# Performance work log

Hardware: AMD Instinct MI355X
Metric: run time of the kernel (lower is better)

The kernel has to match this reference:

```python
import jax, jax.numpy as jnp
import numpy as np
import math

B, C, H, W = 64, 32, 80, 80
HEADS, HD = 8, 4
L = H * W
INV_PI = 1.0 / math.pi


def _conv2d(x, w, pad):
    return jax.lax.conv_general_dilated(x, w, (1, 1), pad, dimension_numbers=('NCHW', 'OIHW', 'NCHW'))


def _lin_angular(x, qkv_w, proj_w, proj_b, dconv_w):
    # x: (B, L, C) -> softmax-free angular linear attention
    qkv = (x @ qkv_w.T).reshape(B, L, 3, HEADS, HD).transpose(2, 0, 3, 1, 4)
    q, k, v = qkv[0], qkv[1], qkv[2]  # (B, HEADS, L, HD)
    q = q / jnp.linalg.norm(q, axis=-1, keepdims=True)
    k = k / jnp.linalg.norm(k, axis=-1, keepdims=True)
    # depthwise conv over L with kernel (9,1), one channel per head
    dconv_v = jax.lax.conv_general_dilated(v, dconv_w, (1, 1), ((4, 4), (0, 0)),
                                           feature_group_count=HEADS,
                                           dimension_numbers=('NCHW', 'OIHW', 'NCHW'))
    attn = jnp.einsum('bhld,bhle->bhde', k, v)  # (B,H,HD,HD)
    out = 0.5 * v + INV_PI * jnp.einsum('bhld,bhde->bhle', q, attn)
    out = out / jnp.linalg.norm(out, axis=-1, keepdims=True)
    out = out + dconv_v
    out = out.transpose(0, 2, 1, 3).reshape(B, L, C)
    return out @ proj_w.T + proj_b


def _xca(x, qkv_w, temp, proj_w, proj_b):
    # x: (B, L, C) -> cross-covariance (channel) attention
    qkv = (x @ qkv_w.T).reshape(B, L, 3, HEADS, HD).transpose(2, 0, 3, 4, 1)
    q, k, v = qkv[0], qkv[1], qkv[2]  # (B, HEADS, HD, L)
    q = q / jnp.maximum(jnp.linalg.norm(q, axis=-1, keepdims=True), 1e-12)
    k = k / jnp.maximum(jnp.linalg.norm(k, axis=-1, keepdims=True), 1e-12)
    attn = jax.nn.softmax(jnp.einsum('bhdn,bhen->bhde', q, k) * temp, axis=-1)
    out = jnp.einsum('bhde,bhen->bhdn', attn, v)  # (B,H,HD,L)
    out = out.transpose(0, 3, 1, 2).reshape(B, L, C)
    return out @ proj_w.T + proj_b


def _chan_vec(f, wa, ba, wa2, ba2, wm, bm, wm2, bm2):
    # f: (B, C, L) -> (B, C, 1) pooled channel descriptor (avg + max branches)
    avg = f.mean(axis=-1)  # (B, C)
    mx = f.max(axis=-1)    # (B, C)
    a = jax.nn.relu(avg @ wa.T + ba) @ wa2.T + ba2
    m = jax.nn.relu(mx @ wm.T + bm) @ wm2.T + bm2
    return (a + m)[..., None]  # (B, C, 1)


def _spatial_gate(a, c1w, c1b, c2w, c2b):
    # a: (B, C, L) -> (B, 1, L) softmax spatial gate
    am = a.reshape(B, C, H, W)
    pooled = jnp.concatenate([am.mean(axis=1, keepdims=True), am.max(axis=1, keepdims=True)], axis=1)
    y = jax.nn.relu(_conv2d(pooled, c1w, ((1, 1), (1, 1))) + c1b[None, :, None, None])
    y = _conv2d(y, c2w, ((1, 1), (1, 1))) + c2b[None, :, None, None]
    return jax.nn.softmax(y.reshape(B, 1, L), axis=-1)


def _forward(rgb, freq, la_qkv_w, la_proj_w, la_proj_b, la_dconv_w,
             xa_qkv_w, xa_temp, xa_proj_w, xa_proj_b,
             c1s_w, c1s_b, c2s_w, c2s_b,
             avg1_w, avg1_b, max1_w, max1_b, avg2_w, avg2_b, max2_w, max2_b,
             avg11_w, avg11_b, max11_w, max11_b, avg22_w, avg22_b, max22_w, max22_b):
    x1 = rgb.reshape(B, C, L).transpose(0, 2, 1)  # to_3d: (B, L, C)
    la1 = _lin_angular(x1, la_qkv_w, la_proj_w, la_proj_b, la_dconv_w)
    x2 = freq.reshape(B, C, L).transpose(0, 2, 1)
    xa1 = _xca(x2, xa_qkv_w, xa_temp, xa_proj_w, xa_proj_b)
    # CAFM works on flattened (B, C, L)
    f1 = la1.transpose(0, 2, 1)
    f2 = xa1.transpose(0, 2, 1)
    a1 = _chan_vec(f1, avg1_w, avg1_b, avg11_w, avg11_b, max1_w, max1_b, max11_w, max11_b)
    a2 = _chan_vec(f2, avg2_w, avg2_b, avg22_w, avg22_b, max2_w, max2_b, max22_w, max22_b)
    cross = jnp.einsum('bci,bdi->bcd', a1, a2)  # (B, C, C)
    a1f = jnp.einsum('bcd,bdl->bcl', jax.nn.softmax(cross, axis=-1), f1)
    a2f = jnp.einsum('bcd,bdl->bcl', jax.nn.softmax(cross.transpose(0, 2, 1), axis=-1), f2)
    g1 = _spatial_gate(a1f, c1s_w, c1s_b, c2s_w, c2s_b)
    g2 = _spatial_gate(a2f, c1s_w, c1s_b, c2s_w, c2s_b)
    f1 = f1 * g1 + f1
    f2 = f2 * g2 + f2
    # torch: (B,C,L).transpose(0,1) -> (C,B,L); sum; permute(1,2,0) -> (B,L,C); to_4d -> (B,C,H,W)
    # transposes cancel: equivalent to (f1+f2).reshape(B, C, H, W)
    return (f1 + f2).reshape(B, C, H, W)


def setup_inputs() -> dict:
    key = jax.random.key(0)
    ks = iter(jax.random.split(key, 40))
    def rn(shape, s=0.05):
        return jax.random.normal(next(ks), shape, dtype=jnp.float32) * s
    return dict(
        rgb=jax.random.normal(next(ks), (B, C, H, W), dtype=jnp.float32),
        freq=jax.random.normal(next(ks), (B, C, H, W), dtype=jnp.float32),
        la_qkv_w=rn((3 * C, C)), la_proj_w=rn((C, C)), la_proj_b=jnp.zeros((C,), jnp.float32),
        la_dconv_w=rn((HEADS, 1, 9, 1)),
        xa_qkv_w=rn((3 * C, C)), xa_temp=jnp.ones((HEADS, 1, 1), jnp.float32),
        xa_proj_w=rn((C, C)), xa_proj_b=jnp.zeros((C,), jnp.float32),
        c1s_w=rn((1, 2, 3, 3)), c1s_b=jnp.zeros((1,), jnp.float32),
        c2s_w=rn((1, 1, 3, 3)), c2s_b=jnp.zeros((1,), jnp.float32),
        avg1_w=rn((16, C)), avg1_b=jnp.zeros((16,), jnp.float32),
        max1_w=rn((16, C)), max1_b=jnp.zeros((16,), jnp.float32),
        avg2_w=rn((16, C)), avg2_b=jnp.zeros((16,), jnp.float32),
        max2_w=rn((16, C)), max2_b=jnp.zeros((16,), jnp.float32),
        avg11_w=rn((C, 16)), avg11_b=jnp.zeros((C,), jnp.float32),
        max11_w=rn((C, 16)), max11_b=jnp.zeros((C,), jnp.float32),
        avg22_w=rn((C, 16)), avg22_b=jnp.zeros((C,), jnp.float32),
        max22_w=rn((C, 16)), max22_b=jnp.zeros((C,), jnp.float32),
    )


def reference(rgb, freq, la_qkv_w, la_proj_w, la_proj_b, la_dconv_w,
              xa_qkv_w, xa_temp, xa_proj_w, xa_proj_b,
              c1s_w, c1s_b, c2s_w, c2s_b,
              avg1_w, avg1_b, max1_w, max1_b, avg2_w, avg2_b, max2_w, max2_b,
              avg11_w, avg11_b, max11_w, max11_b, avg22_w, avg22_b, max22_w, max22_b):
    return _forward(rgb, freq, la_qkv_w, la_proj_w, la_proj_b, la_dconv_w,
                    xa_qkv_w, xa_temp, xa_proj_w, xa_proj_b,
                    c1s_w, c1s_b, c2s_w, c2s_b,
                    avg1_w, avg1_b, max1_w, max1_b, avg2_w, avg2_b, max2_w, max2_b,
                    avg11_w, avg11_b, max11_w, max11_b, avg22_w, avg22_b, max22_w, max22_b)
```

## Files before the change

kernel.cpp:

```cpp
#include <hip/hip_runtime.h>

#define BN 64
#define CN 32
#define HEADSN 8
#define HDN 4
#define LN 6400
#define CL (CN*LN)


__device__ __forceinline__ unsigned fenc(float f){
  unsigned u = __float_as_uint(f);
  return (u & 0x80000000u) ? ~u : (u | 0x80000000u);
}
__device__ __forceinline__ float fdec(unsigned u){
  unsigned v = (u & 0x80000000u) ? (u & 0x7FFFFFFFu) : ~u;
  return __uint_as_float(v);
}

template<bool MAXOP>
__device__ __forceinline__ float bfly32(const float* in, int lane, int* chOut){
  const bool h0 = (lane & 1)  != 0, h1 = (lane & 2)  != 0, h2 = (lane & 4) != 0,
             h3 = (lane & 8)  != 0, h4 = (lane & 16) != 0;
  float a[16];
  #pragma unroll
  for (int i = 0; i < 16; ++i){
    float send = h0 ? in[i] : in[i+16];
    float keep = h0 ? in[i+16] : in[i];
    float recv = __shfl_xor(send, 1, 64);
    a[i] = MAXOP ? fmaxf(keep, recv) : keep + recv;
  }
  float b[8];
  #pragma unroll
  for (int i = 0; i < 8; ++i){
    float send = h1 ? a[i] : a[i+8];
    float keep = h1 ? a[i+8] : a[i];
    float recv = __shfl_xor(send, 2, 64);
    b[i] = MAXOP ? fmaxf(keep, recv) : keep + recv;
  }
  float c[4];
  #pragma unroll
  for (int i = 0; i < 4; ++i){
    float send = h2 ? b[i] : b[i+4];
    float keep = h2 ? b[i+4] : b[i];
    float recv = __shfl_xor(send, 4, 64);
    c[i] = MAXOP ? fmaxf(keep, recv) : keep + recv;
  }
  float d[2];
  #pragma unroll
  for (int i = 0; i < 2; ++i){
    float send = h3 ? c[i] : c[i+2];
    float keep = h3 ? c[i+2] : c[i];
    float recv = __shfl_xor(send, 8, 64);
    d[i] = MAXOP ? fmaxf(keep, recv) : keep + recv;
  }
  float e;
  {
    float send = h4 ? d[0] : d[1];
    float keep = h4 ? d[1] : d[0];
    float recv = __shfl_xor(send, 16, 64);
    e = MAXOP ? fmaxf(keep, recv) : keep + recv;
  }
  {
    float recv = __shfl_xor(e, 32, 64);
    e = MAXOP ? fmaxf(e, recv) : e + recv;
  }
  *chOut = (h0?16:0)|(h1?8:0)|(h2?4:0)|(h3?2:0)|(h4?1:0);
  return e;
}

__device__ __forceinline__ float bfly16_sum(const float* in, int lane, int* chOut){
  const bool h0 = (lane & 1) != 0, h1 = (lane & 2) != 0, h2 = (lane & 4) != 0,
             h3 = (lane & 8) != 0;
  float a[8];
  #pragma unroll
  for (int i = 0; i < 8; ++i){
    float send = h0 ? in[i] : in[i+8];
    float keep = h0 ? in[i+8] : in[i];
    float recv = __shfl_xor(send, 1, 64);
    a[i] = keep + recv;
  }
  float b[4];
  #pragma unroll
  for (int i = 0; i < 4; ++i){
    float send = h1 ? a[i] : a[i+4];
    float keep = h1 ? a[i+4] : a[i];
    float recv = __shfl_xor(send, 2, 64);
    b[i] = keep + recv;
  }
  float c[2];
  #pragma unroll
  for (int i = 0; i < 2; ++i){
    float send = h2 ? b[i] : b[i+2];
    float keep = h2 ? b[i+2] : b[i];
    float recv = __shfl_xor(send, 4, 64);
    c[i] = keep + recv;
  }
  float e;
  {
    float send = h3 ? c[0] : c[1];
    float keep = h3 ? c[1] : c[0];
    float recv = __shfl_xor(send, 8, 64);
    e = keep + recv;
  }
  e += __shfl_xor(e, 16, 64);
  e += __shfl_xor(e, 32, 64);
  *chOut = (h0?8:0)|(h1?4:0)|(h2?2:0)|(h3?1:0);
  return e;
}

__global__ __launch_bounds__(256, 4) void k_la_reduce(const float* __restrict__ rgb,
                                                      const float* __restrict__ Wqkv,
                                                      float* __restrict__ la_attn){
  __shared__ float2 xs2[256*17];
  const int b = blockIdx.y, l0 = blockIdx.x*256, tid = threadIdx.x;
  const float* xg = rgb + (size_t)b*CL + l0;
  #pragma unroll
  for (int c2 = 0; c2 < 16; ++c2){
    float e0 = xg[(2*c2)*LN + tid];
    float e1 = xg[(2*c2+1)*LN + tid];
    xs2[tid*17 + c2] = make_float2(e0, e1);
  }
  __syncthreads();
  const int wave = __builtin_amdgcn_readfirstlane(tid >> 6);
  const int lane = tid & 63;
  const float* Wk = Wqkv + (32 + wave*8)*32;
  const float* Wv = Wqkv + (64 + wave*8)*32;
  float acc[32];
  #pragma unroll
  for (int i = 0; i < 32; ++i) acc[i] = 0.f;
  for (int it = 0; it < 4; ++it){
    const int ll = it*64 + lane;
    float xv[32];
    #pragma unroll
    for (int c2 = 0; c2 < 16; ++c2){
      float2 t = xs2[ll*17 + c2];
      xv[2*c2] = t.x; xv[2*c2+1] = t.y;
    }
    float kk[8], vv[8];
    #pragma unroll
    for (int r = 0; r < 8; ++r){ kk[r] = 0.f; vv[r] = 0.f; }
    #pragma unroll
    for (int c = 0; c < 32; ++c){
      #pragma unroll
      for (int r = 0; r < 8; ++r){
        kk[r] = fmaf(Wk[r*32 + c], xv[c], kk[r]);
        vv[r] = fmaf(Wv[r*32 + c], xv[c], vv[r]);
      }
    }
    #pragma unroll
    for (int hh = 0; hh < 2; ++hh){
      const float* k = kk + hh*4;
      const float* v = vv + hh*4;
      float rn = rsqrtf(k[0]*k[0] + k[1]*k[1] + k[2]*k[2] + k[3]*k[3]);
      #pragma unroll
      for (int d = 0; d < 4; ++d){
        float kn = k[d]*rn;
        #pragma unroll
        for (int e = 0; e < 4; ++e)
          acc[hh*16 + d*4 + e] = fmaf(kn, v[e], acc[hh*16 + d*4 + e]);
      }
    }
  }
  int ch;
  float s = bfly32<false>(acc, lane, &ch);
  if (lane < 32) atomicAdd(la_attn + b*128 + wave*32 + ch, s);
}

__global__ __launch_bounds__(256, 4) void k_xa_reduce(const float* __restrict__ freq,
                                                      const float* __restrict__ Wqkv,
                                                      float* __restrict__ xa_sums){
  __shared__ float2 xs2[256*17];
  const int b = blockIdx.y, l0 = blockIdx.x*256, tid = threadIdx.x;
  const float* xg = freq + (size_t)b*CL + l0;
  #pragma unroll
  for (int c2 = 0; c2 < 16; ++c2){
    float e0 = xg[(2*c2)*LN + tid];
    float e1 = xg[(2*c2+1)*LN + tid];
    xs2[tid*17 + c2] = make_float2(e0, e1);
  }
  __syncthreads();
  const int wave = __builtin_amdgcn_readfirstlane(tid >> 6);
  const int lane = tid & 63;
  const float* Wq = Wqkv + (0  + wave*8)*32;
  const float* Wk = Wqkv + (32 + wave*8)*32;
  float acc[48];
  #pragma unroll
  for (int i = 0; i < 48; ++i) acc[i] = 0.f;
  for (int it = 0; it < 4; ++it){
    const int ll = it*64 + lane;
    float xv[32];
    #pragma unroll
    for (int c2 = 0; c2 < 16; ++c2){
      float2 t = xs2[ll*17 + c2];
      xv[2*c2] = t.x; xv[2*c2+1] = t.y;
    }
    float qq[8], kk[8];
    #pragma unroll
    for (int r = 0; r < 8; ++r){ qq[r] = 0.f; kk[r] = 0.f; }
    #pragma unroll
    for (int c = 0; c < 32; ++c){
      #pragma unroll
      for (int r = 0; r < 8; ++r){
        qq[r] = fmaf(Wq[r*32 + c], xv[c], qq[r]);
        kk[r] = fmaf(Wk[r*32 + c], xv[c], kk[r]);
      }
    }
    #pragma unroll
    for (int hh = 0; hh < 2; ++hh){
      const float* q = qq + hh*4;
      const float* k = kk + hh*4;
      const int base = hh*24;
      #pragma unroll
      for (int d = 0; d < 4; ++d){
        #pragma unroll
        for (int e = 0; e < 4; ++e)
          acc[base + d*4 + e] = fmaf(q[d], k[e], acc[base + d*4 + e]);
      }
      #pragma unroll
      for (int d = 0; d < 4; ++d) acc[base + 16 + d] = fmaf(q[d], q[d], acc[base + 16 + d]);
      #pragma unroll
      for (int e = 0; e < 4; ++e) acc[base + 20 + e] = fmaf(k[e], k[e], acc[base + 20 + e]);
    }
  }
  float* dst = xa_sums + b*192 + wave*48;
  int ch;
  float s0 = bfly32<false>(acc, lane, &ch);
  if (lane < 32) atomicAdd(dst + ch, s0);
  int ch2;
  float s1 = bfly16_sum(acc + 32, lane, &ch2);
  if (lane < 16) atomicAdd(dst + 32 + ch2, s1);
}

__global__ __launch_bounds__(64) void k_fold(const float* __restrict__ xa_sums,
                                             const float* __restrict__ temp,
                                             const float* __restrict__ Wqkv,
                                             const float* __restrict__ Wp,
                                             float* __restrict__ M2){
  __shared__ float attn_s[128];
  const int b = blockIdx.x, t = threadIdx.x;
  if (t < 32){
    const int h = t >> 2, d = t & 3;
    const float* xss = xa_sums + b*192 + h*24;
    const float tmp = temp[h];
    const float nq = fmaxf(sqrtf(xss[16 + d]), 1e-12f);
    float lg[4]; float m = -1e30f;
    #pragma unroll
    for (int e = 0; e < 4; ++e){
      float nk = fmaxf(sqrtf(xss[20 + e]), 1e-12f);
      lg[e] = xss[d*4 + e] * tmp / (nq*nk);
      m = fmaxf(m, lg[e]);
    }
    float Z = 0.f;
    #pragma unroll
    for (int e = 0; e < 4; ++e){ lg[e] = __expf(lg[e] - m); Z += lg[e]; }
    float iZ = 1.f/Z;
    #pragma unroll
    for (int e = 0; e < 4; ++e) attn_s[h*16 + d*4 + e] = lg[e]*iZ;
  }
  __syncthreads();
  if (t < 32){
    const int c = t;
    const float* Wv = Wqkv + 64*32;
    float tmpv[32];
    #pragma unroll
    for (int k = 0; k < 32; ++k){
      const int h = k >> 2, d = k & 3;
      float s = 0.f;
      #pragma unroll
      for (int e = 0; e < 4; ++e)
        s = fmaf(attn_s[h*16 + d*4 + e], Wv[(h*4 + e)*32 + c], s);
      tmpv[k] = s;
    }
    float out[32];
    #pragma unroll
    for (int r = 0; r < 32; ++r) out[r] = 0.f;
    #pragma unroll
    for (int k = 0; k < 32; ++k){
      #pragma unroll
      for (int r = 0; r < 32; ++r)
        out[r] = fmaf(Wp[r*32 + k], tmpv[k], out[r]);
    }
    #pragma unroll
    for (int r = 0; r < 32; ++r) M2[b*1024 + r*32 + c] = out[r];
  }
}

__global__ __launch_bounds__(256, 4) void k_la_final(const float* __restrict__ rgb,
    const float* __restrict__ Wqkv, const float* __restrict__ la_attn,
    const float* __restrict__ dconv_w, const float* __restrict__ Wp,
    const float* __restrict__ bp, float* __restrict__ f1,
    float* __restrict__ sum1, unsigned* __restrict__ max1e){
  __shared__ float2 vsh2[264*17];
  const int b = blockIdx.y, l0 = blockIdx.x*256, tid = threadIdx.x;
  const int l = l0 + tid, lane = tid & 63;
  const float* xg = rgb + (size_t)b*CL;
  float x[32];
  #pragma unroll
  for (int c = 0; c < 32; ++c) x[c] = xg[c*LN + l];
  {
    float v[32];
    #pragma unroll
    for (int r = 0; r < 32; ++r) v[r] = 0.f;
    const float* Wv = Wqkv + 64*32;
    #pragma unroll
    for (int c = 0; c < 32; ++c){
      #pragma unroll
      for (int r = 0; r < 32; ++r) v[r] = fmaf(Wv[r*32 + c], x[c], v[r]);
    }
    #pragma unroll
    for (int c2 = 0; c2 < 16; ++c2)
      vsh2[(tid+4)*17 + c2] = make_float2(v[2*c2], v[2*c2+1]);
  }
  if (tid < 128){
    const int p = tid >> 4, c2 = tid & 15;
    const int hl  = (p < 4) ? (l0 - 4 + p) : (l0 + 252 + p);
    const int pos = (p < 4) ? p : (256 + p);
    float2 vh = make_float2(0.f, 0.f);
    if (hl >= 0 && hl < LN){
      const float* W0 = Wqkv + (64 + 2*c2)*32;
      #pragma unroll 8
      for (int cc = 0; cc < 32; ++cc){
        float xv = xg[cc*LN + hl];
        vh.x = fmaf(W0[cc],      xv, vh.x);
        vh.y = fmaf(W0[32 + cc], xv, vh.y);
      }
    }
    vsh2[pos*17 + c2] = vh;
  }
  __syncthreads();
  float y[32];
  #pragma unroll
  for (int h = 0; h < 8; ++h){
    float q0 = 0.f, q1 = 0.f, q2 = 0.f, q3 = 0.f;
    const float* Wq = Wqkv + h*4*32;
    #pragma unroll
    for (int c = 0; c < 32; ++c){
      q0 = fmaf(Wq[c],      x[c], q0);
      q1 = fmaf(Wq[32 + c], x[c], q1);
      q2 = fmaf(Wq[64 + c], x[c], q2);
      q3 = fmaf(Wq[96 + c], x[c], q3);
    }
    const float rnq = rsqrtf(q0*q0 + q1*q1 + q2*q2 + q3*q3);
    q0 *= rnq; q1 *= rnq; q2 *= rnq; q3 *= rnq;
    const float* at = la_attn + b*128 + h*16;
    const float2 v01 = vsh2[(tid+4)*17 + h*2];
    const float2 v23 = vsh2[(tid+4)*17 + h*2 + 1];
    const float vo[4] = {v01.x, v01.y, v23.x, v23.y};
    float o[4]; float ss = 0.f;
    #pragma unroll
    for (int e = 0; e < 4; ++e){
      float t = 0.f;
      t = fmaf(q0, at[e],      t);
      t = fmaf(q1, at[4 + e],  t);
      t = fmaf(q2, at[8 + e],  t);
      t = fmaf(q3, at[12 + e], t);
      o[e] = fmaf(0.31830988618379067f, t, 0.5f*vo[e]);
      ss = fmaf(o[e], o[e], ss);
    }
    const float rno = rsqrtf(ss);
    float dc[4] = {0.f, 0.f, 0.f, 0.f};
    #pragma unroll
    for (int j = 0; j < 9; ++j){
      const float w = dconv_w[h*9 + j];
      const float2 p0 = vsh2[(tid + j)*17 + h*2];
      const float2 p1 = vsh2[(tid + j)*17 + h*2 + 1];
      dc[0] = fmaf(w, p0.x, dc[0]);
      dc[1] = fmaf(w, p0.y, dc[1]);
      dc[2] = fmaf(w, p1.x, dc[2]);
      dc[3] = fmaf(w, p1.y, dc[3]);
    }
    #pragma unroll
    for (int e = 0; e < 4; ++e) y[h*4 + e] = fmaf(o[e], rno, dc[e]);
  }
  float vals[32];
  float* f1p = f1 + (size_t)b*CL + l;
  #pragma unroll
  for (int r = 0; r < 32; ++r){
    float val = bp[r];
    #pragma unroll
    for (int c = 0; c < 32; ++c) val = fmaf(Wp[r*32 + c], y[c], val);
    f1p[r*LN] = val;
    vals[r] = val;
  }
  int ch;
  float s = bfly32<false>(vals, lane, &ch);
  float m = bfly32<true >(vals, lane, &ch);
  if (lane < 32){
    atomicAdd(&sum1[b*32 + ch], s);
    atomicMax(&max1e[b*32 + ch], fenc(m));
  }
}

__global__ __launch_bounds__(256, 4) void k_xa_final(const float* __restrict__ freq,
    const float* __restrict__ M2, const float* __restrict__ bp,
    float* __restrict__ f2, float* __restrict__ sum2, unsigned* __restrict__ max2e){
  const int b = blockIdx.y, l0 = blockIdx.x*256, tid = threadIdx.x;
  const int l = l0 + tid, lane = tid & 63;
  const float* xg = freq + (size_t)b*CL;
  float x[32];
  #pragma unroll
  for (int c = 0; c < 32; ++c) x[c] = xg[c*LN + l];
  const float* M = M2 + b*1024;
  float vals[32];
  #pragma unroll
  for (int r = 0; r < 32; ++r) vals[r] = bp[r];
  #pragma unroll
  for (int c = 0; c < 32; ++c){
    #pragma unroll
    for (int r = 0; r < 32; ++r) vals[r] = fmaf(M[r*32 + c], x[c], vals[r]);
  }
  float* f2p = f2 + (size_t)b*CL + l;
  #pragma unroll
  for (int r = 0; r < 32; ++r) f2p[r*LN] = vals[r];
  int ch;
  float s = bfly32<false>(vals, lane, &ch);
  float m = bfly32<true >(vals, lane, &ch);
  if (lane < 32){
    atomicAdd(&sum2[b*32 + ch], s);
    atomicMax(&max2e[b*32 + ch], fenc(m));
  }
}

__global__ __launch_bounds__(64) void k_vec(
  const float* __restrict__ sum1, const unsigned* __restrict__ max1e,
  const float* __restrict__ sum2, const unsigned* __restrict__ max2e,
  const float* __restrict__ a1w, const float* __restrict__ a1b,
  const float* __restrict__ m1w, const float* __restrict__ m1b,
  const float* __restrict__ a2w, const float* __restrict__ a2b,
  const float* __restrict__ m2w, const float* __restrict__ m2b,
  const float* __restrict__ a11w, const float* __restrict__ a11b,
  const float* __restrict__ m11w, const float* __restrict__ m11b,
  const float* __restrict__ a22w, const float* __restrict__ a22b,
  const float* __restrict__ m22w, const float* __restrict__ m22b,
  float* __restrict__ w1o, float* __restrict__ w2o){
  __shared__ float avg1[32], mx1[32], avg2[32], mx2[32];
  __shared__ float h_a1[16], h_m1[16], h_a2[16], h_m2[16];
  __shared__ float a1v[32], a2v[32];
  const int b = blockIdx.x, t = threadIdx.x;
  if (t < 32){
    avg1[t] = sum1[b*32 + t] * (1.f/6400.f);
    mx1[t]  = fdec(max1e[b*32 + t]);
    avg2[t] = sum2[b*32 + t] * (1.f/6400.f);
    mx2[t]  = fdec(max2e[b*32 + t]);
  }
  __syncthreads();
  if (t < 16){
    float s1 = a1b[t], s2 = m1b[t], s3 = a2b[t], s4 = m2b[t];
    for (int c = 0; c < 32; ++c){
      s1 = fmaf(avg1[c], a1w[t*32 + c], s1);
      s2 = fmaf(mx1[c],  m1w[t*32 + c], s2);
      s3 = fmaf(avg2[c], a2w[t*32 + c], s3);
      s4 = fmaf(mx2[c],  m2w[t*32 + c], s4);
    }
    h_a1[t] = fmaxf(s1, 0.f); h_m1[t] = fmaxf(s2, 0.f);
    h_a2[t] = fmaxf(s3, 0.f); h_m2[t] = fmaxf(s4, 0.f);
  }
  __syncthreads();
  if (t < 32){
    float v1 = a11b[t] + m11b[t];
    float v2 = a22b[t] + m22b[t];
    for (int k = 0; k < 16; ++k){
      v1 += h_a1[k]*a11w[t*16 + k] + h_m1[k]*m11w[t*16 + k];
      v2 += h_a2[k]*a22w[t*16 + k] + h_m2[k]*m22w[t*16 + k];
    }
    a1v[t] = v1; a2v[t] = v2;
  }
  __syncthreads();
  if (t < 32){
    float s = a1v[t], m = -1e30f;
    for (int d = 0; d < 32; ++d) m = fmaxf(m, s*a2v[d]);
    float Z = 0.f;
    for (int d = 0; d < 32; ++d) Z += __expf(s*a2v[d] - m);
    float iZ = 1.f/Z;
    for (int d = 0; d < 32; ++d) w1o[b*1024 + t*32 + d] = __expf(s*a2v[d] - m)*iZ;
    float s2 = a2v[t]; m = -1e30f;
    for (int d = 0; d < 32; ++d) m = fmaxf(m, s2*a1v[d]);
    Z = 0.f;
    for (int d = 0; d < 32; ++d) Z += __expf(s2*a1v[d] - m);
    iZ = 1.f/Z;
    for (int d = 0; d < 32; ++d) w2o[b*1024 + t*32 + d] = __expf(s2*a1v[d] - m)*iZ;
  }
}

__global__ __launch_bounds__(256, 4) void k_mix(const float* __restrict__ f1,
    const float* __restrict__ f2, const float* __restrict__ w1,
    const float* __restrict__ w2, float* __restrict__ pooled1,
    float* __restrict__ pooled2){
  const int b = blockIdx.y, l = blockIdx.x*256 + threadIdx.x;
  float fv[32], av[32];
  {
    const float* f1p = f1 + (size_t)b*CL + l;
    #pragma unroll
    for (int d = 0; d < 32; ++d) fv[d] = f1p[d*LN];
    const float* W = w1 + b*1024;
    #pragma unroll
    for (int c = 0; c < 32; ++c) av[c] = 0.f;
    #pragma unroll
    for (int d = 0; d < 32; ++d){
      #pragma unroll
      for (int c = 0; c < 32; ++c) av[c] = fmaf(W[c*32 + d], fv[d], av[c]);
    }
    float s = 0.f, m = -1e30f;
    #pragma unroll
    for (int c = 0; c < 32; ++c){ s += av[c]; m = fmaxf(m, av[c]); }
    pooled1[(size_t)b*2*LN + l]      = s*(1.f/32.f);
    pooled1[(size_t)b*2*LN + LN + l] = m;
  }
  {
    const float* f2p = f2 + (size_t)b*CL + l;
    #pragma unroll
    for (int d = 0; d < 32; ++d) fv[d] = f2p[d*LN];
    const float* W = w2 + b*1024;
    #pragma unroll
    for (int c = 0; c < 32; ++c) av[c] = 0.f;
    #pragma unroll
    for (int d = 0; d < 32; ++d){
      #pragma unroll
      for (int c = 0; c < 32; ++c) av[c] = fmaf(W[c*32 + d], fv[d], av[c]);
    }
    float s = 0.f, m = -1e30f;
    #pragma unroll
    for (int c = 0; c < 32; ++c){ s += av[c]; m = fmaxf(m, av[c]); }
    pooled2[(size_t)b*2*LN + l]      = s*(1.f/32.f);
    pooled2[(size_t)b*2*LN + LN + l] = m;
  }
}

__global__ __launch_bounds__(256) void k_gate(const float* __restrict__ pooled1,
    const float* __restrict__ pooled2, const float* __restrict__ c1w,
    const float* __restrict__ c1b, const float* __restrict__ c2w,
    const float* __restrict__ c2b, float* __restrict__ g1, float* __restrict__ g2){
  __shared__ float y1s[6400];
  __shared__ float red[8];
  const int b = blockIdx.y, t = blockIdx.x, tid = threadIdx.x;
  const float* src = (t == 0 ? pooled1 : pooled2) + (size_t)b*2*LN;
  float* dst = (t == 0 ? g1 : g2) + (size_t)b*LN;
  for (int i = tid; i < 6400; i += 256){
    const int yy = i/80, xx = i - yy*80;
    float a = c1b[0];
    #pragma unroll
    for (int ky = 0; ky < 3; ++ky){
      const int y2 = yy + ky - 1;
      if (y2 < 0 || y2 >= 80) continue;
      #pragma unroll
      for (int kx = 0; kx < 3; ++kx){
        const int x2 = xx + kx - 1;
        if (x2 < 0 || x2 >= 80) continue;
        const int j = y2*80 + x2;
        a = fmaf(src[j],        c1w[ky*3 + kx],     a);
        a = fmaf(src[6400 + j], c1w[9 + ky*3 + kx], a);
      }
    }
    y1s[i] = fmaxf(a, 0.f);
  }
  __syncthreads();
  float y2r[25]; float lmax = -1e30f;
  #pragma unroll
  for (int ii = 0; ii < 25; ++ii){
    const int i = tid + ii*256;
    const int yy = i/80, xx = i - yy*80;
    float a = c2b[0];
    #pragma unroll
    for (int ky = 0; ky < 3; ++ky){
      const int y2 = yy + ky - 1;
      if (y2 < 0 || y2 >= 80) continue;
      #pragma unroll
      for (int kx = 0; kx < 3; ++kx){
        const int x2 = xx + kx - 1;
        if (x2 < 0 || x2 >= 80) continue;
        a = fmaf(y1s[y2*80 + x2], c2w[ky*3 + kx], a);
      }
    }
    y2r[ii] = a; lmax = fmaxf(lmax, a);
  }
  #pragma unroll
  for (int off = 32; off >= 1; off >>= 1) lmax = fmaxf(lmax, __shfl_xor(lmax, off, 64));
  if ((tid & 63) == 0) red[tid >> 6] = lmax;
  __syncthreads();
  const float bmax = fmaxf(fmaxf(red[0], red[1]), fmaxf(red[2], red[3]));
  float lsum = 0.f;
  #pragma unroll
  for (int ii = 0; ii < 25; ++ii){
    float e = __expf(y2r[ii] - bmax);
    y2r[ii] = e; lsum += e;
  }
  #pragma unroll
  for (int off = 32; off >= 1; off >>= 1) lsum += __shfl_xor(lsum, off, 64);
  if ((tid & 63) == 0) red[4 + (tid >> 6)] = lsum;
  __syncthreads();
  const float inv = 1.f/(red[4] + red[5] + red[6] + red[7]);
  #pragma unroll
  for (int ii = 0; ii < 25; ++ii) dst[tid + ii*256] = y2r[ii]*inv;
}

__global__ __launch_bounds__(256) void k_final(const float* __restrict__ f1,
    const float* __restrict__ f2, const float* __restrict__ g1,
    const float* __restrict__ g2, float* __restrict__ out){
  const int i = blockIdx.x*256 + threadIdx.x;
  const int flat = i*4;
  const int b = flat / CL;
  const int rem = flat - b*CL;
  const int l = rem % LN;
  const float4 a  = *(const float4*)(f1 + flat);
  const float4 c  = *(const float4*)(f2 + flat);
  const float4 ga = *(const float4*)(g1 + b*LN + l);
  const float4 gc = *(const float4*)(g2 + b*LN + l);
  float4 o;
  o.x = fmaf(a.x, ga.x, a.x) + fmaf(c.x, gc.x, c.x);
  o.y = fmaf(a.y, ga.y, a.y) + fmaf(c.y, gc.y, c.y);
  o.z = fmaf(a.z, ga.z, a.z) + fmaf(c.z, gc.z, c.z);
  o.w = fmaf(a.w, ga.w, a.w) + fmaf(c.w, gc.w, c.w);
  *(float4*)(out + flat) = o;
}

extern "C" void kernel_launch(void* const* d_in, const int* in_sizes, int n_in,
                              void* d_out, int out_size, void* d_ws, size_t ws_size,
                              hipStream_t stream){
  const float* rgb     = (const float*)d_in[0];
  const float* freq    = (const float*)d_in[1];
  const float* la_qkv  = (const float*)d_in[2];
  const float* la_pw   = (const float*)d_in[3];
  const float* la_pb   = (const float*)d_in[4];
  const float* la_dw   = (const float*)d_in[5];
  const float* xa_qkv  = (const float*)d_in[6];
  const float* xa_temp = (const float*)d_in[7];
  const float* xa_pw   = (const float*)d_in[8];
  const float* xa_pb   = (const float*)d_in[9];
  const float* c1w     = (const float*)d_in[10];
  const float* c1b     = (const float*)d_in[11];
  const float* c2w     = (const float*)d_in[12];
  const float* c2b     = (const float*)d_in[13];

  float* ws = (float*)d_ws;
  size_t o = 0;
  float* f1      = ws + o; o += (size_t)BN*CL;
  float* f2      = ws + o; o += (size_t)BN*CL;
  float* la_attn = ws + o; o += BN*128;
  float* xa_sums = ws + o; o += BN*192;
  float* sum1    = ws + o; o += BN*32;
  unsigned* max1e = (unsigned*)(ws + o); o += BN*32;
  float* sum2    = ws + o; o += BN*32;
  unsigned* max2e = (unsigned*)(ws + o); o += BN*32;
  float* w1      = ws + o; o += BN*1024;
  float* w2      = ws + o; o += BN*1024;
  float* pooled1 = ws + o; o += (size_t)BN*2*LN;
  float* pooled2 = ws + o; o += (size_t)BN*2*LN;
  float* g1      = ws + o; o += (size_t)BN*LN;
  float* g2      = ws + o; o += (size_t)BN*LN;
  float* M2      = ws + o; o += (size_t)BN*1024;

  const size_t nz = (size_t)BN*128 + BN*192 + (size_t)BN*32*4;
  hipMemsetAsync(la_attn, 0, nz*sizeof(float), stream);

  k_la_reduce<<<dim3(25, BN), 256, 0, stream>>>(rgb, la_qkv, la_attn);
  k_xa_reduce<<<dim3(25, BN), 256, 0, stream>>>(freq, xa_qkv, xa_sums);
  k_fold     <<<BN, 64, 0, stream>>>(xa_sums, xa_temp, xa_qkv, xa_pw, M2);
  k_la_final <<<dim3(25, BN), 256, 0, stream>>>(rgb, la_qkv, la_attn, la_dw, la_pw, la_pb,
                                                f1, sum1, max1e);
  k_xa_final <<<dim3(25, BN), 256, 0, stream>>>(freq, M2, xa_pb, f2, sum2, max2e);
  k_vec<<<BN, 64, 0, stream>>>(sum1, max1e, sum2, max2e,
      (const float*)d_in[14], (const float*)d_in[15], (const float*)d_in[16], (const float*)d_in[17],
      (const float*)d_in[18], (const float*)d_in[19], (const float*)d_in[20], (const float*)d_in[21],
      (const float*)d_in[22], (const float*)d_in[23], (const float*)d_in[24], (const float*)d_in[25],
      (const float*)d_in[26], (const float*)d_in[27], (const float*)d_in[28], (const float*)d_in[29],
      w1, w2);
  k_mix  <<<dim3(25, BN), 256, 0, stream>>>(f1, f2, w1, w2, pooled1, pooled2);
  k_gate <<<dim3(2, BN), 256, 0, stream>>>(pooled1, pooled2, c1w, c1b, c2w, c2b, g1, g2);
  k_final<<<12800, 256, 0, stream>>>(f1, f2, g1, g2, (float*)d_out);
}
```

Baseline: 569.4 us.

## Stage value projection per head pair with double-buffered LDS to raise occupancy

In k_la_final, the V projection for all 32 channels is no longer computed up front and stored in one large shared array. It is now computed 8 channels (two heads) at a time into a small double-buffered shared tile, with halo rows copied from a separate cached halo buffer. This cuts shared memory and live registers so launch bounds can allow 6 blocks per CU instead of 4. The cost is three extra __syncthreads and more interleaved work per stage.

Result: slower. 903.6 us (+58.7%).

```diff
diff --git a/kernel.cpp b/kernel.cpp
--- a/kernel.cpp
+++ b/kernel.cpp
@@ -285,12 +285,13 @@
   }
 }
 
-__global__ __launch_bounds__(256, 4) void k_la_final(const float* __restrict__ rgb,
+__global__ __launch_bounds__(256, 6) void k_la_final(const float* __restrict__ rgb,
     const float* __restrict__ Wqkv, const float* __restrict__ la_attn,
     const float* __restrict__ dconv_w, const float* __restrict__ Wp,
     const float* __restrict__ bp, float* __restrict__ f1,
     float* __restrict__ sum1, unsigned* __restrict__ max1e){
-  __shared__ float2 vsh2[264*17];
+  __shared__ float vt[2*2640];
+  __shared__ float vhalo[8*34];
   const int b = blockIdx.y, l0 = blockIdx.x*256, tid = threadIdx.x;
   const int l = l0 + tid, lane = tid & 63;
   const float* xg = rgb + (size_t)b*CL;
@@ -298,18 +299,20 @@
   #pragma unroll
   for (int c = 0; c < 32; ++c) x[c] = xg[c*LN + l];
   {
-    float v[32];
-    #pragma unroll
-    for (int r = 0; r < 32; ++r) v[r] = 0.f;
     const float* Wv = Wqkv + 64*32;
+    float vv[8];
+    #pragma unroll
+    for (int r = 0; r < 8; ++r) vv[r] = 0.f;
     #pragma unroll
     for (int c = 0; c < 32; ++c){
       #pragma unroll
-      for (int r = 0; r < 32; ++r) v[r] = fmaf(Wv[r*32 + c], x[c], v[r]);
-    }
-    #pragma unroll
-    for (int c2 = 0; c2 < 16; ++c2)
-      vsh2[(tid+4)*17 + c2] = make_float2(v[2*c2], v[2*c2+1]);
+      for (int r = 0; r < 8; ++r) vv[r] = fmaf(Wv[r*32 + c], x[c], vv[r]);
+    }
+    float* vt0 = vt + (tid+4)*10;
+    *(float2*)&vt0[0] = make_float2(vv[0], vv[1]);
+    *(float2*)&vt0[2] = make_float2(vv[2], vv[3]);
+    *(float2*)&vt0[4] = make_float2(vv[4], vv[5]);
+    *(float2*)&vt0[6] = make_float2(vv[6], vv[7]);
   }
   if (tid < 128){
     const int p = tid >> 4, c2 = tid & 15;
@@ -325,52 +328,80 @@
         vh.y = fmaf(W0[32 + cc], xv, vh.y);
       }
     }
-    vsh2[pos*17 + c2] = vh;
+    *(float2*)&vhalo[p*34 + 2*c2] = vh;
+    if (c2 < 4) *(float2*)&vt[pos*10 + 2*c2] = vh;
   }
   __syncthreads();
   float y[32];
   #pragma unroll
-  for (int h = 0; h < 8; ++h){
-    float q0 = 0.f, q1 = 0.f, q2 = 0.f, q3 = 0.f;
-    const float* Wq = Wqkv + h*4*32;
-    #pragma unroll
-    for (int c = 0; c < 32; ++c){
-      q0 = fmaf(Wq[c],      x[c], q0);
-      q1 = fmaf(Wq[32 + c], x[c], q1);
-      q2 = fmaf(Wq[64 + c], x[c], q2);
-      q3 = fmaf(Wq[96 + c], x[c], q3);
-    }
-    const float rnq = rsqrtf(q0*q0 + q1*q1 + q2*q2 + q3*q3);
-    q0 *= rnq; q1 *= rnq; q2 *= rnq; q3 *= rnq;
-    const float* at = la_attn + b*128 + h*16;
-    const float2 v01 = vsh2[(tid+4)*17 + h*2];
-    const float2 v23 = vsh2[(tid+4)*17 + h*2 + 1];
-    const float vo[4] = {v01.x, v01.y, v23.x, v23.y};
-    float o[4]; float ss = 0.f;
-    #pragma unroll
-    for (int e = 0; e < 4; ++e){
-      float t = 0.f;
-      t = fmaf(q0, at[e],      t);
-      t = fmaf(q1, at[4 + e],  t);
-      t = fmaf(q2, at[8 + e],  t);
-      t = fmaf(q3, at[12 + e], t);
-      o[e] = fmaf(0.31830988618379067f, t, 0.5f*vo[e]);
-      ss = fmaf(o[e], o[e], ss);
-    }
-    const float rno = rsqrtf(ss);
-    float dc[4] = {0.f, 0.f, 0.f, 0.f};
-    #pragma unroll
-    for (int j = 0; j < 9; ++j){
-      const float w = dconv_w[h*9 + j];
-      const float2 p0 = vsh2[(tid + j)*17 + h*2];
-      const float2 p1 = vsh2[(tid + j)*17 + h*2 + 1];
-      dc[0] = fmaf(w, p0.x, dc[0]);
-      dc[1] = fmaf(w, p0.y, dc[1]);
-      dc[2] = fmaf(w, p1.x, dc[2]);
-      dc[3] = fmaf(w, p1.y, dc[3]);
-    }
-    #pragma unroll
-    for (int e = 0; e < 4; ++e) y[h*4 + e] = fmaf(o[e], rno, dc[e]);
+  for (int s = 0; s < 4; ++s){
+    const float* vtc = vt + (s & 1)*2640;
+    #pragma unroll
+    for (int hp = 0; hp < 2; ++hp){
+      const int h = s*2 + hp;
+      float q0 = 0.f, q1 = 0.f, q2 = 0.f, q3 = 0.f;
+      const float* Wq = Wqkv + h*4*32;
+      #pragma unroll
+      for (int c = 0; c < 32; ++c){
+        q0 = fmaf(Wq[c],      x[c], q0);
+        q1 = fmaf(Wq[32 + c], x[c], q1);
+        q2 = fmaf(Wq[64 + c], x[c], q2);
+        q3 = fmaf(Wq[96 + c], x[c], q3);
+      }
+      const float rnq = rsqrtf(q0*q0 + q1*q1 + q2*q2 + q3*q3);
+      q0 *= rnq; q1 *= rnq; q2 *= rnq; q3 *= rnq;
+      const float* at = la_attn + b*128 + h*16;
+      const float2 v01 = *(const float2*)&vtc[(tid+4)*10 + hp*4];
+      const float2 v23 = *(const float2*)&vtc[(tid+4)*10 + hp*4 + 2];
+      const float vo[4] = {v01.x, v01.y, v23.x, v23.y};
+      float o[4]; float ss = 0.f;
+      #pragma unroll
+      for (int e = 0; e < 4; ++e){
+        float t = 0.f;
+        t = fmaf(q0, at[e],      t);
+        t = fmaf(q1, at[4 + e],  t);
+        t = fmaf(q2, at[8 + e],  t);
+        t = fmaf(q3, at[12 + e], t);
+        o[e] = fmaf(0.31830988618379067f, t, 0.5f*vo[e]);
+        ss = fmaf(o[e], o[e], ss);
+      }
+      const float rno = rsqrtf(ss);
+      float dc[4] = {0.f, 0.f, 0.f, 0.f};
+      #pragma unroll
+      for (int j = 0; j < 9; ++j){
+        const float w = dconv_w[h*9 + j];
+        const float2 p0 = *(const float2*)&vtc[(tid + j)*10 + hp*4];
+        const float2 p1 = *(const float2*)&vtc[(tid + j)*10 + hp*4 + 2];
+        dc[0] = fmaf(w, p0.x, dc[0]);
+        dc[1] = fmaf(w, p0.y, dc[1]);
+        dc[2] = fmaf(w, p1.x, dc[2]);
+        dc[3] = fmaf(w, p1.y, dc[3]);
+      }
+      #pragma unroll
+      for (int e = 0; e < 4; ++e) y[h*4 + e] = fmaf(o[e], rno, dc[e]);
+    }
+    if (s < 3){
+      const float* Wvn = Wqkv + (64 + (s+1)*8)*32;
+      float vv[8];
+      #pragma unroll
+      for (int r = 0; r < 8; ++r) vv[r] = 0.f;
+      #pragma unroll
+      for (int c = 0; c < 32; ++c){
+        #pragma unroll
+        for (int r = 0; r < 8; ++r) vv[r] = fmaf(Wvn[r*32 + c], x[c], vv[r]);
+      }
+      float* vtn = vt + ((s+1) & 1)*2640 + (tid+4)*10;
+      *(float2*)&vtn[0] = make_float2(vv[0], vv[1]);
+      *(float2*)&vtn[2] = make_float2(vv[2], vv[3]);
+      *(float2*)&vtn[4] = make_float2(vv[4], vv[5]);
+      *(float2*)&vtn[6] = make_float2(vv[6], vv[7]);
+      if (tid < 64){
+        const int px = tid >> 3, e = tid & 7;
+        const int pos = (px < 4) ? px : (256 + px);
+        vt[((s+1) & 1)*2640 + pos*10 + e] = vhalo[px*34 + (s+1)*8 + e];
+      }
+      __syncthreads();
+    }
   }
   float vals[32];
   float* f1p = f1 + (size_t)b*CL + l;
```
